# Performance work log

Measured on AMD Instinct MI355X. Metric: run time of the kernel, lower is better.

Reference implementation:

```python
import jax, jax.numpy as jnp
import numpy as np

B, S, D_MODEL, D_OUT = 4, 4096, 512, 64


def setup_inputs() -> dict:
    key = jax.random.key(0)
    ks = jax.random.split(key, 10)
    query = jax.random.normal(ks[0], (B, S, D_MODEL), dtype=jnp.float32)
    key_t = jax.random.normal(ks[1], (B, S, D_MODEL), dtype=jnp.float32)
    value = jax.random.normal(ks[2], (B, S, D_MODEL), dtype=jnp.float32)
    mask = jax.random.randint(ks[3], (B, S, S), 0, 2, dtype=jnp.int32)
    sc = 1.0 / np.sqrt(D_MODEL)
    Wq = jax.random.uniform(ks[4], (D_MODEL, D_OUT), minval=-sc, maxval=sc, dtype=jnp.float32)
    bq = jnp.zeros((D_OUT,), dtype=jnp.float32)
    Wk = jax.random.uniform(ks[5], (D_MODEL, D_OUT), minval=-sc, maxval=sc, dtype=jnp.float32)
    bk = jnp.zeros((D_OUT,), dtype=jnp.float32)
    Wv = jax.random.uniform(ks[6], (D_MODEL, D_OUT), minval=-sc, maxval=sc, dtype=jnp.float32)
    bv = jnp.zeros((D_OUT,), dtype=jnp.float32)
    return {"query": query, "key": key_t, "value": value, "mask": mask,
            "Wq": Wq, "bq": bq, "Wk": Wk, "bk": bk, "Wv": Wv, "bv": bv}


def reference(query, key, value, mask, Wq, bq, Wk, bk, Wv, bv):
    # Linear projections (single head): [B,S,D_MODEL] @ [D_MODEL,D_OUT] + bias
    q = jnp.einsum('bsd,de->bse', query, Wq) + bq
    k = jnp.einsum('bsd,de->bse', key, Wk) + bk
    v = jnp.einsum('bsd,de->bse', value, Wv) + bv
    dim_k = k.shape[-1]
    scores = jnp.einsum('bqe,bke->bqk', q, k) / jnp.sqrt(jnp.float32(dim_k))  # [B,S,S]
    scores = jnp.where(mask == 0, -jnp.inf, scores)
    weights = jax.nn.softmax(scores, axis=-1)
    # dropout is identity in eval mode / for deterministic reference
    outputs = jnp.einsum('bqk,bke->bqe', weights, v)  # [B,S,D_OUT]
    return outputs
```

## Files before the change

### kernel.cpp

```cpp
#include <hip/hip_runtime.h>
#include <hip/hip_bf16.h>

#define BB 4
#define SS 4096
#define DMODEL 512
#define DOUT 64

typedef __bf16 bf16_t;
typedef __bf16 bf16x8 __attribute__((ext_vector_type(8)));
typedef float floatx4 __attribute__((ext_vector_type(4)));

__global__ __launch_bounds__(256) void wtrans_kernel(
    const float* __restrict__ Wq, const float* __restrict__ Wk,
    const float* __restrict__ Wv, bf16_t* __restrict__ wT) {
  int idx = blockIdx.x * 256 + threadIdx.x;
  int mat = idx >> 12;
  int r   = idx & 4095;
  int e   = r & 63;
  int d0  = (r >> 6) << 3;
  const float* W = (mat == 0) ? Wq : ((mat == 1) ? Wk : Wv);
  bf16_t* dst = wT + (size_t)mat * (DOUT * DMODEL) + (size_t)e * DMODEL + d0;
#pragma unroll
  for (int j = 0; j < 8; ++j) dst[j] = (bf16_t)W[(size_t)(d0 + j) * DOUT + e];
}

__global__ __launch_bounds__(256) void proj_kernel(
    const float* __restrict__ inq, const float* __restrict__ ink,
    const float* __restrict__ inv, const bf16_t* __restrict__ wT,
    const float* __restrict__ bq, const float* __restrict__ bk,
    const float* __restrict__ bv,
    bf16_t* __restrict__ q_ws, bf16_t* __restrict__ k_ws,
    bf16_t* __restrict__ v_wsT) {
  const int mat = blockIdx.x >> 8;
  const int s0  = (blockIdx.x & 255) << 6;
  const int lane = threadIdx.x & 63;
  const int w    = threadIdx.x >> 6;
  const int col  = lane & 15, quad = lane >> 4;

  const float* inp  = (mat == 0) ? inq : ((mat == 1) ? ink : inv);
  const float* bias = (mat == 0) ? bq : ((mat == 1) ? bk : bv);
  const bf16_t* wt  = wT + (size_t)mat * (DOUT * DMODEL);

  const int arow = s0 + w * 16 + col;
  floatx4 acc[4] = {};

  for (int ch = 0; ch < 16; ++ch) {
    const int d0 = ch * 32 + quad * 8;
    float4 a0 = *(const float4*)(inp + (size_t)arow * DMODEL + d0);
    float4 a1 = *(const float4*)(inp + (size_t)arow * DMODEL + d0 + 4);
    bf16x8 af;
    af[0] = (bf16_t)a0.x; af[1] = (bf16_t)a0.y; af[2] = (bf16_t)a0.z; af[3] = (bf16_t)a0.w;
    af[4] = (bf16_t)a1.x; af[5] = (bf16_t)a1.y; af[6] = (bf16_t)a1.z; af[7] = (bf16_t)a1.w;
#pragma unroll
    for (int c = 0; c < 4; ++c) {
      bf16x8 bw = *(const bf16x8*)(wt + (size_t)(c * 16 + col) * DMODEL + d0);
      acc[c] = __builtin_amdgcn_mfma_f32_16x16x32_bf16(af, bw, acc[c], 0, 0, 0);
    }
  }

#pragma unroll
  for (int c = 0; c < 4; ++c) {
    float bcol = bias[c * 16 + col];
#pragma unroll
    for (int r = 0; r < 4; ++r) {
      int row = s0 + w * 16 + quad * 4 + r;
      float v = acc[c][r] + bcol;
      if (mat == 2) {
        int b = row >> 12, sp = row & 4095;
        v_wsT[((size_t)(b * DOUT + c * 16 + col)) * SS + sp] = (bf16_t)v;
      } else {
        bf16_t* dst = (mat == 0) ? q_ws : k_ws;
        dst[(size_t)row * DOUT + c * 16 + col] = (bf16_t)v;
      }
    }
  }
}

__global__ __launch_bounds__(256) void attn_kernel(
    const bf16_t* __restrict__ q_ws, const bf16_t* __restrict__ k_ws,
    const bf16_t* __restrict__ v_wsT, const int* __restrict__ mask,
    float* __restrict__ out) {
  const int b  = blockIdx.x >> 6;
  const int q0 = (blockIdx.x & 63) << 6;
  const int lane = threadIdx.x & 63;
  const int w    = threadIdx.x >> 6;
  const int col  = lane & 15, quad = lane >> 4;

  __shared__ bf16_t Plds[64][72];

  const int qrowA = q0 + w * 16 + col;
  const bf16_t* qbase = q_ws + ((size_t)(b * SS) + qrowA) * DOUT + quad * 8;
  const bf16x8 qa0 = *(const bf16x8*)(qbase);
  const bf16x8 qa1 = *(const bf16x8*)(qbase + 32);

  const int* mrow = mask + ((size_t)(b * SS) + qrowA) * SS + quad * 8;

  floatx4 o[4] = {};
  float l_acc = 0.f;

  bf16x8 kc[4][2];
  int4   mc[2][2];

  auto loadK = [&](int k0, bf16x8 kf[4][2]) {
#pragma unroll
    for (int c = 0; c < 4; ++c)
#pragma unroll
      for (int s = 0; s < 2; ++s)
        kf[c][s] = *(const bf16x8*)(k_ws + ((size_t)(b * SS) + k0 + c * 16 + col) * DOUT + s * 32 + quad * 8);
  };
  auto loadM = [&](int k0, int4 m[2][2]) {
#pragma unroll
    for (int s = 0; s < 2; ++s) {
      const int4* mp = (const int4*)(mrow + k0 + s * 32);
      m[s][0] = mp[0];
      m[s][1] = mp[1];
    }
  };

  loadK(0, kc);
  loadM(0, mc);

  const bf16_t* prow_r = &Plds[w * 16 + col][quad * 8];

  for (int k0 = 0; k0 < SS; k0 += 64) {
    const int k0n = (k0 + 64 < SS) ? k0 + 64 : k0;
    bf16x8 kn[4][2];
    int4   mn[2][2];
    loadK(k0n, kn);
    loadM(k0n, mn);

    bf16x8 vc[4][2];
#pragma unroll
    for (int c = 0; c < 4; ++c)
#pragma unroll
      for (int s = 0; s < 2; ++s)
        vc[c][s] = *(const bf16x8*)(v_wsT + ((size_t)(b * DOUT) + c * 16 + col) * SS + k0 + s * 32 + quad * 8);

    floatx4 sacc[4];
#pragma unroll
    for (int c = 0; c < 4; ++c) {
      floatx4 z = {};
      z = __builtin_amdgcn_mfma_f32_16x16x32_bf16(qa0, kc[c][0], z, 0, 0, 0);
      z = __builtin_amdgcn_mfma_f32_16x16x32_bf16(qa1, kc[c][1], z, 0, 0, 0);
      sacc[c] = z;
    }

#pragma unroll
    for (int c = 0; c < 4; ++c)
#pragma unroll
      for (int r = 0; r < 4; ++r)
        Plds[w * 16 + quad * 4 + r][c * 16 + col] = (bf16_t)__expf(sacc[c][r] * 0.125f);

    asm volatile("s_waitcnt lgkmcnt(0)" ::: "memory");

    bf16x8 pa0 = *(const bf16x8*)(prow_r);
    bf16x8 pa1 = *(const bf16x8*)(prow_r + 32);

    float lp = 0.f;
    bf16x8 pm0, pm1;
    auto apply = [&](bf16x8 pa, int4 mlo, int4 mhi, bf16x8& pm) {
      int mm[8] = {mlo.x, mlo.y, mlo.z, mlo.w, mhi.x, mhi.y, mhi.z, mhi.w};
#pragma unroll
      for (int j = 0; j < 8; ++j) {
        bf16_t pv = (mm[j] != 0) ? pa[j] : (bf16_t)0.0f;
        pm[j] = pv;
        lp += (float)pv;
      }
    };
    apply(pa0, mc[0][0], mc[0][1], pm0);
    apply(pa1, mc[1][0], mc[1][1], pm1);
    lp += __shfl_xor(lp, 16);
    lp += __shfl_xor(lp, 32);
    l_acc += lp;

#pragma unroll
    for (int c = 0; c < 4; ++c) {
      o[c] = __builtin_amdgcn_mfma_f32_16x16x32_bf16(pm0, vc[c][0], o[c], 0, 0, 0);
      o[c] = __builtin_amdgcn_mfma_f32_16x16x32_bf16(pm1, vc[c][1], o[c], 0, 0, 0);
    }

#pragma unroll
    for (int c = 0; c < 4; ++c) { kc[c][0] = kn[c][0]; kc[c][1] = kn[c][1]; }
    mc[0][0] = mn[0][0]; mc[0][1] = mn[0][1];
    mc[1][0] = mn[1][0]; mc[1][1] = mn[1][1];
  }

#pragma unroll
  for (int r = 0; r < 4; ++r) {
    float lr = __shfl(l_acc, quad * 4 + r, 64);
    float inv_l = 1.0f / lr;
    int row = q0 + w * 16 + quad * 4 + r;
#pragma unroll
    for (int c = 0; c < 4; ++c)
      out[((size_t)(b * SS) + row) * DOUT + c * 16 + col] = o[c][r] * inv_l;
  }
}

extern "C" void kernel_launch(void* const* d_in, const int* in_sizes, int n_in,
                              void* d_out, int out_size, void* d_ws, size_t ws_size,
                              hipStream_t stream) {
  const float* query = (const float*)d_in[0];
  const float* key   = (const float*)d_in[1];
  const float* value = (const float*)d_in[2];
  const int*   mask  = (const int*)d_in[3];
  const float* Wq = (const float*)d_in[4];
  const float* bq = (const float*)d_in[5];
  const float* Wk = (const float*)d_in[6];
  const float* bk = (const float*)d_in[7];
  const float* Wv = (const float*)d_in[8];
  const float* bv = (const float*)d_in[9];
  float* out = (float*)d_out;

  bf16_t* q_ws  = (bf16_t*)d_ws;
  bf16_t* k_ws  = q_ws + (size_t)BB * SS * DOUT;
  bf16_t* v_wsT = k_ws + (size_t)BB * SS * DOUT;
  bf16_t* wT    = v_wsT + (size_t)BB * SS * DOUT;

  hipLaunchKernelGGL(wtrans_kernel, dim3(48), dim3(256), 0, stream, Wq, Wk, Wv, wT);
  hipLaunchKernelGGL(proj_kernel, dim3(768), dim3(256), 0, stream,
                     query, key, value, wT, bq, bk, bv, q_ws, k_ws, v_wsT);
  hipLaunchKernelGGL(attn_kernel, dim3(256), dim3(256), 0, stream,
                     q_ws, k_ws, v_wsT, mask, out);
}
```

Measured before the change: 506.7 us.

## Split key range across four wave groups per attention block with LDS reduction

The attention kernel grows from 4 to 16 waves per block. The waves form four groups, and each group handles an interleaved quarter of the key/mask tiles for the same 64 query rows. Partial output accumulators and row sums are then reduced through a shared LDS arena that reuses the P buffers. The aim is to hide mask and K/V load latency, since the old launch ran only one 4-wave block per CU. In exchange it drops the software prefetch of K, adds two block barriers and a reduction epilogue, and raises register and LDS pressure.

Result: slower. 517.7 us (+2.2%).

```diff
diff --git a/kernel.cpp b/kernel.cpp
--- a/kernel.cpp
+++ b/kernel.cpp
@@ -5,6 +5,7 @@
 #define SS 4096
 #define DMODEL 512
 #define DOUT 64
+#define KSPLIT 4
 
 typedef __bf16 bf16_t;
 typedef __bf16 bf16x8 __attribute__((ext_vector_type(8)));
@@ -76,38 +77,33 @@
   }
 }
 
-__global__ __launch_bounds__(256) void attn_kernel(
+__global__ __launch_bounds__(1024, 4) void attn_kernel(
     const bf16_t* __restrict__ q_ws, const bf16_t* __restrict__ k_ws,
     const bf16_t* __restrict__ v_wsT, const int* __restrict__ mask,
     float* __restrict__ out) {
   const int b  = blockIdx.x >> 6;
   const int q0 = (blockIdx.x & 63) << 6;
   const int lane = threadIdx.x & 63;
-  const int w    = threadIdx.x >> 6;
+  const int wv   = threadIdx.x >> 6;
+  const int g    = wv >> 2;
+  const int wi   = wv & 3;
   const int col  = lane & 15, quad = lane >> 4;
 
-  __shared__ bf16_t Plds[64][72];
-
-  const int qrowA = q0 + w * 16 + col;
+  __shared__ __align__(16) char arena[3 * 64 * 66 * 4 + 3 * 64 * 4];
+  bf16_t (*Pg)[72] = (bf16_t (*)[72])(arena + (size_t)g * 64 * 72 * 2);
+  float* Ored = (float*)arena;
+  float* lred = (float*)(arena + 3 * 64 * 66 * 4);
+
+  const int qrowA = q0 + wi * 16 + col;
   const bf16_t* qbase = q_ws + ((size_t)(b * SS) + qrowA) * DOUT + quad * 8;
   const bf16x8 qa0 = *(const bf16x8*)(qbase);
   const bf16x8 qa1 = *(const bf16x8*)(qbase + 32);
-
   const int* mrow = mask + ((size_t)(b * SS) + qrowA) * SS + quad * 8;
 
   floatx4 o[4] = {};
   float l_acc = 0.f;
 
-  bf16x8 kc[4][2];
-  int4   mc[2][2];
-
-  auto loadK = [&](int k0, bf16x8 kf[4][2]) {
-#pragma unroll
-    for (int c = 0; c < 4; ++c)
-#pragma unroll
-      for (int s = 0; s < 2; ++s)
-        kf[c][s] = *(const bf16x8*)(k_ws + ((size_t)(b * SS) + k0 + c * 16 + col) * DOUT + s * 32 + quad * 8);
-  };
+  int4 mc[2][2], mn[2][2];
   auto loadM = [&](int k0, int4 m[2][2]) {
 #pragma unroll
     for (int s = 0; s < 2; ++s) {
@@ -116,18 +112,32 @@
       m[s][1] = mp[1];
     }
   };
-
-  loadK(0, kc);
-  loadM(0, mc);
-
-  const bf16_t* prow_r = &Plds[w * 16 + col][quad * 8];
-
-  for (int k0 = 0; k0 < SS; k0 += 64) {
-    const int k0n = (k0 + 64 < SS) ? k0 + 64 : k0;
-    bf16x8 kn[4][2];
-    int4   mn[2][2];
-    loadK(k0n, kn);
+  loadM(g * 64, mc);
+
+  const bf16_t* prow_r = &Pg[wi * 16 + col][quad * 8];
+
+  const int NIT = SS / (64 * KSPLIT);
+  for (int it = 0; it < NIT; ++it) {
+    const int k0 = g * 64 + it * (64 * KSPLIT);
+    const int k0n = (it + 1 < NIT) ? k0 + 64 * KSPLIT : k0;
     loadM(k0n, mn);
+
+    floatx4 sacc[4];
+    {
+      bf16x8 kc[4][2];
+#pragma unroll
+      for (int c = 0; c < 4; ++c)
+#pragma unroll
+        for (int s = 0; s < 2; ++s)
+          kc[c][s] = *(const bf16x8*)(k_ws + ((size_t)(b * SS) + k0 + c * 16 + col) * DOUT + s * 32 + quad * 8);
+#pragma unroll
+      for (int c = 0; c < 4; ++c) {
+        floatx4 z = {};
+        z = __builtin_amdgcn_mfma_f32_16x16x32_bf16(qa0, kc[c][0], z, 0, 0, 0);
+        z = __builtin_amdgcn_mfma_f32_16x16x32_bf16(qa1, kc[c][1], z, 0, 0, 0);
+        sacc[c] = z;
+      }
+    }
 
     bf16x8 vc[4][2];
 #pragma unroll
@@ -136,20 +146,11 @@
       for (int s = 0; s < 2; ++s)
         vc[c][s] = *(const bf16x8*)(v_wsT + ((size_t)(b * DOUT) + c * 16 + col) * SS + k0 + s * 32 + quad * 8);
 
-    floatx4 sacc[4];
-#pragma unroll
-    for (int c = 0; c < 4; ++c) {
-      floatx4 z = {};
-      z = __builtin_amdgcn_mfma_f32_16x16x32_bf16(qa0, kc[c][0], z, 0, 0, 0);
-      z = __builtin_amdgcn_mfma_f32_16x16x32_bf16(qa1, kc[c][1], z, 0, 0, 0);
-      sacc[c] = z;
-    }
-
 #pragma unroll
     for (int c = 0; c < 4; ++c)
 #pragma unroll
       for (int r = 0; r < 4; ++r)
-        Plds[w * 16 + quad * 4 + r][c * 16 + col] = (bf16_t)__expf(sacc[c][r] * 0.125f);
+        Pg[wi * 16 + quad * 4 + r][c * 16 + col] = (bf16_t)__expf(sacc[c][r] * 0.125f);
 
     asm volatile("s_waitcnt lgkmcnt(0)" ::: "memory");
 
@@ -179,20 +180,42 @@
       o[c] = __builtin_amdgcn_mfma_f32_16x16x32_bf16(pm1, vc[c][1], o[c], 0, 0, 0);
     }
 
-#pragma unroll
-    for (int c = 0; c < 4; ++c) { kc[c][0] = kn[c][0]; kc[c][1] = kn[c][1]; }
     mc[0][0] = mn[0][0]; mc[0][1] = mn[0][1];
     mc[1][0] = mn[1][0]; mc[1][1] = mn[1][1];
   }
 
-#pragma unroll
-  for (int r = 0; r < 4; ++r) {
-    float lr = __shfl(l_acc, quad * 4 + r, 64);
-    float inv_l = 1.0f / lr;
-    int row = q0 + w * 16 + quad * 4 + r;
+  __syncthreads();
+  if (g > 0) {
+    float* Og = Ored + (size_t)(g - 1) * 64 * 66;
 #pragma unroll
     for (int c = 0; c < 4; ++c)
-      out[((size_t)(b * SS) + row) * DOUT + c * 16 + col] = o[c][r] * inv_l;
+#pragma unroll
+      for (int r = 0; r < 4; ++r)
+        Og[(wi * 16 + quad * 4 + r) * 66 + c * 16 + col] = o[c][r];
+    if (quad == 0) lred[(g - 1) * 64 + wi * 16 + col] = l_acc;
+  }
+  __syncthreads();
+  if (g == 0) {
+#pragma unroll
+    for (int p = 0; p < 3; ++p) {
+      float* Og = Ored + (size_t)p * 64 * 66;
+#pragma unroll
+      for (int c = 0; c < 4; ++c)
+#pragma unroll
+        for (int r = 0; r < 4; ++r)
+          o[c][r] += Og[(wi * 16 + quad * 4 + r) * 66 + c * 16 + col];
+    }
+#pragma unroll
+    for (int r = 0; r < 4; ++r) {
+      float lr = __shfl(l_acc, quad * 4 + r, 64);
+#pragma unroll
+      for (int p = 0; p < 3; ++p) lr += lred[p * 64 + wi * 16 + quad * 4 + r];
+      float inv_l = 1.0f / lr;
+      int row = q0 + wi * 16 + quad * 4 + r;
+#pragma unroll
+      for (int c = 0; c < 4; ++c)
+        out[((size_t)(b * SS) + row) * DOUT + c * 16 + col] = o[c][r] * inv_l;
+    }
   }
 }
 
@@ -219,6 +242,6 @@
   hipLaunchKernelGGL(wtrans_kernel, dim3(48), dim3(256), 0, stream, Wq, Wk, Wv, wT);
   hipLaunchKernelGGL(proj_kernel, dim3(768), dim3(256), 0, stream,
                      query, key, value, wT, bq, bk, bv, q_ws, k_ws, v_wsT);
-  hipLaunchKernelGGL(attn_kernel, dim3(256), dim3(256), 0, stream,
+  hipLaunchKernelGGL(attn_kernel, dim3(256), dim3(1024), 0, stream,
                      q_ws, k_ws, v_wsT, mask, out);
 }
```
